# Performance work log

Measured on AMD Instinct MI355X. Metric: run time of the kernel, lower is better.

## Reference

```python
import jax, jax.numpy as jnp
import numpy as np

B, S, D = 4, 2048, 1024
H = 16
HD = D // H  # head dim = 64


def setup_inputs() -> dict:
    key = jax.random.key(0)
    ks = jax.random.split(key, 9)
    s = 1.0 / np.sqrt(D)
    return {
        "Q": jax.random.normal(ks[0], (B, S, D), dtype=jnp.float32),
        "K": jax.random.normal(ks[1], (B, S, D), dtype=jnp.float32),
        "V": jax.random.normal(ks[2], (B, S, D), dtype=jnp.float32),
        "Wq": jax.random.uniform(ks[3], (D, D), jnp.float32, -s, s),
        "bq": jax.random.uniform(ks[4], (D,), jnp.float32, -s, s),
        "Wk": jax.random.uniform(ks[5], (D, D), jnp.float32, -s, s),
        "bk": jax.random.uniform(ks[6], (D,), jnp.float32, -s, s),
        "Wv": jax.random.uniform(ks[7], (D, D), jnp.float32, -s, s),
        "bv": jax.random.uniform(ks[8], (D,), jnp.float32, -s, s),
    }


def reference(Q, K, V, Wq, bq, Wk, bk, Wv, bv):
    # Linear projections, split into heads: (B, H, S, HD)
    def proj(x, W, b):
        y = x @ W + b  # torch Linear uses x @ W.T; here W is stored pre-transposed (D_in, D_out)
        return y.reshape(B, S, H, HD).transpose(0, 2, 1, 3)

    q = proj(Q, Wq, bq)
    k = proj(K, Wk, bk)
    v = proj(V, Wv, bv)

    scale = 1.0 / jnp.sqrt(jnp.float32(HD))
    scores = jnp.einsum("bhqd,bhkd->bhqk", q, k) * scale  # (B,H,S,S)
    # causal mask (mask=True path): -inf above the diagonal
    causal = jnp.triu(jnp.full((S, S), -jnp.inf, dtype=scores.dtype), k=1)
    scores = scores + causal
    attn = jax.nn.softmax(scores, axis=-1)
    ctx = jnp.einsum("bhqk,bhkd->bhqd", attn, v)  # (B,H,S,HD)
    return ctx.transpose(0, 2, 1, 3).reshape(B, S, H * HD)
```

## Files before the change

kernel.cpp:

```cpp
#include <hip/hip_runtime.h>
#include <hip/hip_bf16.h>
#include <stdint.h>

#define B_  4
#define S_  2048
#define D_  1024
#define H_  16
#define HD_ 64
#define LOG2E 1.44269504088896f

typedef unsigned short u16;
typedef short bf16x8 __attribute__((ext_vector_type(8)));
typedef float f32x4 __attribute__((ext_vector_type(4)));

static __device__ __forceinline__ u16 f2bf(float f) {
    union { float f; uint32_t u; } v; v.f = f;
    return (u16)((v.u + 0x7FFF + ((v.u >> 16) & 1)) >> 16);
}

static __device__ __forceinline__ uint32_t cvt_pk_bf16(float lo, float hi) {
    uint32_t r;
    asm("v_cvt_pk_bf16_f32 %0, %1, %2" : "=v"(r) : "v"(lo), "v"(hi));
    return r;
}

static __device__ __forceinline__ uint32_t pk2(float lo, float hi) {
    return __builtin_amdgcn_perm(__float_as_uint(hi), __float_as_uint(lo), 0x07060302u);
}

static __device__ __forceinline__ bf16x8 rd_swz(const u16* base, int row, int slot) {
    return *(const bf16x8*)((const char*)base + row * 128 + ((slot ^ (row & 7)) << 4));
}

static __device__ __forceinline__ void gll_swz(const u16* grow0, size_t stride,
                                               u16* lds_chunk, int lane) {
    const int r = lane >> 3;
    const int slot = (lane & 7) ^ r;
    const u16* g = grow0 + (size_t)r * stride + slot * 8;
    __builtin_amdgcn_global_load_lds(
        (const __attribute__((address_space(1))) uint32_t*)g,
        (__attribute__((address_space(3))) uint32_t*)lds_chunk, 16, 0, 0);
}

__global__ __launch_bounds__(256) void wtrans(
    const float* __restrict__ W0, const float* __restrict__ W1, const float* __restrict__ W2,
    u16* __restrict__ T0, u16* __restrict__ T1, u16* __restrict__ T2)
{
    const float* W = blockIdx.z == 0 ? W0 : (blockIdx.z == 1 ? W1 : W2);
    u16* T       = blockIdx.z == 0 ? T0 : (blockIdx.z == 1 ? T1 : T2);
    __shared__ float t[32][33];
    const int n0 = blockIdx.x * 32, k0 = blockIdx.y * 32;
    const int tx = threadIdx.x, ty = threadIdx.y;
#pragma unroll
    for (int i = 0; i < 4; ++i)
        t[ty + i * 8][tx] = W[(size_t)(k0 + ty + i * 8) * D_ + n0 + tx];
    __syncthreads();
#pragma unroll
    for (int i = 0; i < 4; ++i)
        T[(size_t)(n0 + ty + i * 8) * D_ + k0 + tx] = f2bf(t[tx][ty + i * 8]);
}

template <int MODE>
__global__ __launch_bounds__(256) void proj_gemm(
    const float* __restrict__ X, const u16* __restrict__ Wt,
    const float* __restrict__ bias, u16* __restrict__ out)
{
    __shared__ __align__(16) u16 lA[2][128 * 64];
    __shared__ __align__(16) u16 lB[2][128 * 64];
    const int tid = threadIdx.x;
    const int m0 = blockIdx.x * 128, n0 = blockIdx.y * 128;
    const int w = tid >> 6, lane = tid & 63;
    const int lr = lane & 15, lg = lane >> 4;
    const int wr = (w >> 1) * 64, wc = (w & 1) * 64;

    f32x4 acc[4][4] = {};
    float4 areg[8];

    auto loadA = [&](int k0) {
#pragma unroll
        for (int i = 0; i < 4; ++i) {
            const int lin = (i * 256 + tid) * 8;
            const int r = lin >> 6, c = lin & 63;
            const float* p = X + (size_t)(m0 + r) * D_ + k0 + c;
            areg[2 * i]     = *(const float4*)p;
            areg[2 * i + 1] = *(const float4*)(p + 4);
        }
    };
    auto writeA = [&](u16* dst) {
#pragma unroll
        for (int i = 0; i < 4; ++i) {
            const int lin = (i * 256 + tid) * 8;
            const int r = lin >> 6, c = lin & 63;
            uint4 pk;
            pk.x = pk2(areg[2 * i].x,     areg[2 * i].y);
            pk.y = pk2(areg[2 * i].z,     areg[2 * i].w);
            pk.z = pk2(areg[2 * i + 1].x, areg[2 * i + 1].y);
            pk.w = pk2(areg[2 * i + 1].z, areg[2 * i + 1].w);
            const int phys = r * 128 + (((c >> 3) ^ (r & 7)) << 4);
            *(uint4*)((char*)dst + phys) = pk;
        }
    };
    auto stageB = [&](int k0, u16* dst) {
#pragma unroll
        for (int i = 0; i < 4; ++i) {
            const int c = w * 4 + i;
            gll_swz(Wt + (size_t)(n0 + c * 8) * D_ + k0, D_, dst + c * 512, lane);
        }
    };
    auto mfmaStep = [&](const u16* A, const u16* Bb) {
#pragma unroll
        for (int kk = 0; kk < 2; ++kk) {
            bf16x8 af[4], bfr[4];
#pragma unroll
            for (int m = 0; m < 4; ++m)
                af[m] = rd_swz(A, wr + m * 16 + lr, kk * 4 + lg);
#pragma unroll
            for (int n = 0; n < 4; ++n)
                bfr[n] = rd_swz(Bb, wc + n * 16 + lr, kk * 4 + lg);
#pragma unroll
            for (int m = 0; m < 4; ++m)
#pragma unroll
                for (int n = 0; n < 4; ++n)
                    acc[m][n] = __builtin_amdgcn_mfma_f32_16x16x32_bf16(af[m], bfr[n], acc[m][n], 0, 0, 0);
        }
    };

    loadA(0);
    stageB(0, lB[0]);
    writeA(lA[0]);
    __syncthreads();

    for (int k0 = 0, s = 0; k0 < D_; k0 += 64, s ^= 1) {
        const int nk = k0 + 64;
        if (nk < D_) {
            loadA(nk);
            stageB(nk, lB[s ^ 1]);
        }
        mfmaStep(lA[s], lB[s]);
        if (nk < D_) writeA(lA[s ^ 1]);
        __syncthreads();
    }

#pragma unroll
    for (int m = 0; m < 4; ++m)
#pragma unroll
        for (int n = 0; n < 4; ++n)
#pragma unroll
            for (int j = 0; j < 4; ++j) {
                const int gm = m0 + wr + m * 16 + lg * 4 + j;
                const int gn = n0 + wc + n * 16 + lr;
                float y = acc[m][n][j] + bias[gn];
                if (MODE == 0) y *= 0.125f * LOG2E;
                const int bb = gm >> 11, s2 = gm & (S_ - 1);
                const int h = gn >> 6, hd = gn & 63;
                size_t off;
                if (MODE < 2) off = (((size_t)bb * H_ + h) * S_ + s2) * HD_ + hd;
                else {
                    const int s6 = s2 & 63;
                    const int sp = (s2 & ~63) | (s6 & 0x20) | ((s6 & 0xC) << 1) |
                                   ((s6 & 0x10) >> 2) | (s6 & 3);
                    off = (((size_t)bb * H_ + h) * HD_ + hd) * S_ + sp;
                }
                out[off] = f2bf(y);
            }
}

__global__ __launch_bounds__(512) void attn_kernel(
    const u16* __restrict__ qb, const u16* __restrict__ kb,
    const u16* __restrict__ vtb, float* __restrict__ out)
{
    const int bh = blockIdx.y;
    const int b = bh >> 4, h = bh & 15;
    const int tid = threadIdx.x;
    const int w = tid >> 6, lane = tid & 63;
    const int lr = lane & 15, lg = lane >> 4;

    __shared__ __align__(16) u16 lds[2][4][64 * 64];

    const size_t kbase = (size_t)bh * S_ * HD_;
    const size_t vbase = (size_t)bh * HD_ * S_;

    union { uint32_t u[4]; bf16x8 v; } onesf;
    onesf.u[0] = onesf.u[1] = onesf.u[2] = onesf.u[3] = 0x3F803F80u;

    for (int e = 0; e < 2; ++e) {
        const int qi = (e == 0) ? (int)blockIdx.x : 15 - (int)blockIdx.x;
        const int q0 = qi * 128;
        const int qrow = q0 + w * 16 + lr;

        const size_t qoff = ((size_t)bh * S_ + qrow) * HD_;
        const bf16x8 qf0 = *(const bf16x8*)(qb + qoff + lg * 8);
        const bf16x8 qf1 = *(const bf16x8*)(qb + qoff + 32 + lg * 8);

        f32x4 oacc[4] = {};
        f32x4 lacc = {};

        const int tmax = 2 * qi + 1;

        auto stage = [&](int tp, int s) {
            const int kvA = tp * 64, kvB = kvA + 64;
            u16* d = &lds[s][0][0];
            gll_swz(kb + kbase + (size_t)(kvA + w * 8) * HD_, HD_, d + w * 512, lane);
            gll_swz(vtb + vbase + (size_t)(w * 8) * S_ + kvA, S_, d + 4096 + w * 512, lane);
            gll_swz(kb + kbase + (size_t)(kvB + w * 8) * HD_, HD_, d + 8192 + w * 512, lane);
            gll_swz(vtb + vbase + (size_t)(w * 8) * S_ + kvB, S_, d + 12288 + w * 512, lane);
        };

        auto compute = [&](int t, const u16* lK, const u16* lV) {
            const int kv0 = t * 64;
            f32x4 sacc[4];
            __builtin_amdgcn_s_setprio(1);
#pragma unroll
            for (int n = 0; n < 4; ++n) {
                const bf16x8 k0f = rd_swz(lK, n * 16 + lr, lg);
                const bf16x8 k1f = rd_swz(lK, n * 16 + lr, 4 + lg);
                f32x4 z = {};
                z = __builtin_amdgcn_mfma_f32_16x16x32_bf16(k0f, qf0, z, 0, 0, 0);
                z = __builtin_amdgcn_mfma_f32_16x16x32_bf16(k1f, qf1, z, 0, 0, 0);
                sacc[n] = z;
            }
            __builtin_amdgcn_s_setprio(0);

            if (t >= tmax - 1) {
#pragma unroll
                for (int n = 0; n < 4; ++n)
#pragma unroll
                    for (int j = 0; j < 4; ++j)
                        if (kv0 + n * 16 + lg * 4 + j > qrow) sacc[n][j] = -1e30f;
            }

            uint32_t pw[4][2];
#pragma unroll
            for (int n = 0; n < 4; ++n)
#pragma unroll
                for (int jh = 0; jh < 2; ++jh)
                    pw[n][jh] = cvt_pk_bf16(exp2f(sacc[n][2 * jh]),
                                            exp2f(sacc[n][2 * jh + 1]));

            union { uint32_t u[4]; bf16x8 v; } a0, a1;
            a0.u[0] = pw[0][0]; a0.u[1] = pw[0][1];
            a0.u[2] = pw[1][0]; a0.u[3] = pw[1][1];
            a1.u[0] = pw[2][0]; a1.u[1] = pw[2][1];
            a1.u[2] = pw[3][0]; a1.u[3] = pw[3][1];

            __builtin_amdgcn_s_setprio(1);
#pragma unroll
            for (int n = 0; n < 4; ++n) {
                const int row = n * 16 + lr;
                const bf16x8 vf0 = rd_swz(lV, row, lg);
                const bf16x8 vf1 = rd_swz(lV, row, 4 + lg);
                oacc[n] = __builtin_amdgcn_mfma_f32_16x16x32_bf16(a0.v, vf0, oacc[n], 0, 0, 0);
                oacc[n] = __builtin_amdgcn_mfma_f32_16x16x32_bf16(a1.v, vf1, oacc[n], 0, 0, 0);
            }
            lacc = __builtin_amdgcn_mfma_f32_16x16x32_bf16(a0.v, onesf.v, lacc, 0, 0, 0);
            lacc = __builtin_amdgcn_mfma_f32_16x16x32_bf16(a1.v, onesf.v, lacc, 0, 0, 0);
            __builtin_amdgcn_s_setprio(0);
        };

        stage(0, 0);
        __syncthreads();

        for (int tp = 0, s = 0; tp <= tmax; tp += 2, s ^= 1) {
            if (tp + 2 <= tmax) stage(tp + 2, s ^ 1);
            const u16* base = &lds[s][0][0];
            compute(tp, base, base + 4096);
            if (!(tp + 1 == tmax && w < 4)) compute(tp + 1, base + 8192, base + 12288);
            __syncthreads();
        }

        f32x4 inv;
#pragma unroll
        for (int j = 0; j < 4; ++j) inv[j] = 1.f / lacc[j];
#pragma unroll
        for (int j = 0; j < 4; ++j) {
            const int row = q0 + w * 16 + lg * 4 + j;
#pragma unroll
            for (int n = 0; n < 4; ++n)
                out[((size_t)b * S_ + row) * D_ + h * HD_ + n * 16 + lr] = oacc[n][j] * inv[j];
        }
    }
}

extern "C" void kernel_launch(void* const* d_in, const int* in_sizes, int n_in,
                              void* d_out, int out_size, void* d_ws, size_t ws_size,
                              hipStream_t stream) {
    const float* Q  = (const float*)d_in[0];
    const float* K  = (const float*)d_in[1];
    const float* V  = (const float*)d_in[2];
    const float* Wq = (const float*)d_in[3];
    const float* bq = (const float*)d_in[4];
    const float* Wk = (const float*)d_in[5];
    const float* bk = (const float*)d_in[6];
    const float* Wv = (const float*)d_in[7];
    const float* bv = (const float*)d_in[8];
    float* out = (float*)d_out;

    char* ws = (char*)d_ws;
    const size_t WT_BYTES  = (size_t)D_ * D_ * 2;
    const size_t QKV_BYTES = (size_t)B_ * S_ * D_ * 2;
    u16* Wtq = (u16*)(ws);
    u16* Wtk = (u16*)(ws + WT_BYTES);
    u16* Wtv = (u16*)(ws + 2 * WT_BYTES);
    u16* qb  = (u16*)(ws + 3 * WT_BYTES);
    u16* kb  = (u16*)(ws + 3 * WT_BYTES + QKV_BYTES);
    u16* vtb = (u16*)(ws + 3 * WT_BYTES + 2 * QKV_BYTES);

    wtrans<<<dim3(32, 32, 3), dim3(32, 8), 0, stream>>>(Wq, Wk, Wv, Wtq, Wtk, Wtv);
    proj_gemm<0><<<dim3(64, 8), dim3(256), 0, stream>>>(Q, Wtq, bq, qb);
    proj_gemm<1><<<dim3(64, 8), dim3(256), 0, stream>>>(K, Wtk, bk, kb);
    proj_gemm<2><<<dim3(64, 8), dim3(256), 0, stream>>>(V, Wtv, bv, vtb);
    attn_kernel<<<dim3(8, B_ * H_), dim3(512), 0, stream>>>(qb, kb, vtb, out);
}
```

Measured before the change: 150.6 us.

## Share K/V tile loads between both paired query tiles in one pass

Instead of processing the two paired causal query tiles (qi and 15-qi) sequentially, each reloading K/V from global memory, the kernel now streams K/V once up to the longer tile's range and applies each staged tile to both query tiles. This removes the redundant K/V staging for the shorter tile and halves the number of load/sync loop passes. The cost is doubled accumulator registers (two sets of output and row-sum accumulators plus Q fragments), which may raise register pressure and reduce occupancy.

```diff
diff --git a/kernel.cpp b/kernel.cpp
--- a/kernel.cpp
+++ b/kernel.cpp
@@ -183,100 +183,126 @@
     union { uint32_t u[4]; bf16x8 v; } onesf;
     onesf.u[0] = onesf.u[1] = onesf.u[2] = onesf.u[3] = 0x3F803F80u;
 
-    for (int e = 0; e < 2; ++e) {
-        const int qi = (e == 0) ? (int)blockIdx.x : 15 - (int)blockIdx.x;
-        const int q0 = qi * 128;
-        const int qrow = q0 + w * 16 + lr;
-
-        const size_t qoff = ((size_t)bh * S_ + qrow) * HD_;
-        const bf16x8 qf0 = *(const bf16x8*)(qb + qoff + lg * 8);
-        const bf16x8 qf1 = *(const bf16x8*)(qb + qoff + 32 + lg * 8);
-
-        f32x4 oacc[4] = {};
-        f32x4 lacc = {};
-
-        const int tmax = 2 * qi + 1;
-
-        auto stage = [&](int tp, int s) {
-            const int kvA = tp * 64, kvB = kvA + 64;
-            u16* d = &lds[s][0][0];
-            gll_swz(kb + kbase + (size_t)(kvA + w * 8) * HD_, HD_, d + w * 512, lane);
-            gll_swz(vtb + vbase + (size_t)(w * 8) * S_ + kvA, S_, d + 4096 + w * 512, lane);
-            gll_swz(kb + kbase + (size_t)(kvB + w * 8) * HD_, HD_, d + 8192 + w * 512, lane);
-            gll_swz(vtb + vbase + (size_t)(w * 8) * S_ + kvB, S_, d + 12288 + w * 512, lane);
-        };
-
-        auto compute = [&](int t, const u16* lK, const u16* lV) {
-            const int kv0 = t * 64;
-            f32x4 sacc[4];
-            __builtin_amdgcn_s_setprio(1);
-#pragma unroll
-            for (int n = 0; n < 4; ++n) {
-                const bf16x8 k0f = rd_swz(lK, n * 16 + lr, lg);
-                const bf16x8 k1f = rd_swz(lK, n * 16 + lr, 4 + lg);
-                f32x4 z = {};
-                z = __builtin_amdgcn_mfma_f32_16x16x32_bf16(k0f, qf0, z, 0, 0, 0);
-                z = __builtin_amdgcn_mfma_f32_16x16x32_bf16(k1f, qf1, z, 0, 0, 0);
-                sacc[n] = z;
-            }
-            __builtin_amdgcn_s_setprio(0);
-
-            if (t >= tmax - 1) {
-#pragma unroll
-                for (int n = 0; n < 4; ++n)
-#pragma unroll
-                    for (int j = 0; j < 4; ++j)
-                        if (kv0 + n * 16 + lg * 4 + j > qrow) sacc[n][j] = -1e30f;
-            }
-
-            uint32_t pw[4][2];
+    const int qA = (int)blockIdx.x;
+    const int qB = 15 - qA;
+    const int q0A = qA * 128, q0B = qB * 128;
+    const int qrowA = q0A + w * 16 + lr;
+    const int qrowB = q0B + w * 16 + lr;
+    const int tmaxA = 2 * qA + 1, tmaxB = 2 * qB + 1;
+
+    const size_t qoffA = ((size_t)bh * S_ + qrowA) * HD_;
+    const size_t qoffB = ((size_t)bh * S_ + qrowB) * HD_;
+    const bf16x8 qfA0 = *(const bf16x8*)(qb + qoffA + lg * 8);
+    const bf16x8 qfA1 = *(const bf16x8*)(qb + qoffA + 32 + lg * 8);
+    const bf16x8 qfB0 = *(const bf16x8*)(qb + qoffB + lg * 8);
+    const bf16x8 qfB1 = *(const bf16x8*)(qb + qoffB + 32 + lg * 8);
+
+    f32x4 oaccA[4] = {}, oaccB[4] = {};
+    f32x4 laccA = {}, laccB = {};
+
+    auto stage = [&](int tp, int s) {
+        const int kvA = tp * 64, kvB = kvA + 64;
+        u16* d = &lds[s][0][0];
+        gll_swz(kb + kbase + (size_t)(kvA + w * 8) * HD_, HD_, d + w * 512, lane);
+        gll_swz(vtb + vbase + (size_t)(w * 8) * S_ + kvA, S_, d + 4096 + w * 512, lane);
+        gll_swz(kb + kbase + (size_t)(kvB + w * 8) * HD_, HD_, d + 8192 + w * 512, lane);
+        gll_swz(vtb + vbase + (size_t)(w * 8) * S_ + kvB, S_, d + 12288 + w * 512, lane);
+    };
+
+    auto computeT = [&](int t, const u16* lK, const u16* lV,
+                        const bf16x8& Qf0, const bf16x8& Qf1,
+                        f32x4 (&oacc)[4], f32x4& lacc, int qrow, int tmax) {
+        const int kv0 = t * 64;
+        f32x4 sacc[4];
+        __builtin_amdgcn_s_setprio(1);
+#pragma unroll
+        for (int n = 0; n < 4; ++n) {
+            const bf16x8 k0f = rd_swz(lK, n * 16 + lr, lg);
+            const bf16x8 k1f = rd_swz(lK, n * 16 + lr, 4 + lg);
+            f32x4 z = {};
+            z = __builtin_amdgcn_mfma_f32_16x16x32_bf16(k0f, Qf0, z, 0, 0, 0);
+            z = __builtin_amdgcn_mfma_f32_16x16x32_bf16(k1f, Qf1, z, 0, 0, 0);
+            sacc[n] = z;
+        }
+        __builtin_amdgcn_s_setprio(0);
+
+        if (t >= tmax - 1) {
 #pragma unroll
             for (int n = 0; n < 4; ++n)
 #pragma unroll
-                for (int jh = 0; jh < 2; ++jh)
-                    pw[n][jh] = cvt_pk_bf16(exp2f(sacc[n][2 * jh]),
-                                            exp2f(sacc[n][2 * jh + 1]));
-
-            union { uint32_t u[4]; bf16x8 v; } a0, a1;
-            a0.u[0] = pw[0][0]; a0.u[1] = pw[0][1];
-            a0.u[2] = pw[1][0]; a0.u[3] = pw[1][1];
-            a1.u[0] = pw[2][0]; a1.u[1] = pw[2][1];
-            a1.u[2] = pw[3][0]; a1.u[3] = pw[3][1];
-
-            __builtin_amdgcn_s_setprio(1);
-#pragma unroll
-            for (int n = 0; n < 4; ++n) {
-                const int row = n * 16 + lr;
-                const bf16x8 vf0 = rd_swz(lV, row, lg);
-                const bf16x8 vf1 = rd_swz(lV, row, 4 + lg);
-                oacc[n] = __builtin_amdgcn_mfma_f32_16x16x32_bf16(a0.v, vf0, oacc[n], 0, 0, 0);
-                oacc[n] = __builtin_amdgcn_mfma_f32_16x16x32_bf16(a1.v, vf1, oacc[n], 0, 0, 0);
-            }
-            lacc = __builtin_amdgcn_mfma_f32_16x16x32_bf16(a0.v, onesf.v, lacc, 0, 0, 0);
-            lacc = __builtin_amdgcn_mfma_f32_16x16x32_bf16(a1.v, onesf.v, lacc, 0, 0, 0);
-            __builtin_amdgcn_s_setprio(0);
-        };
-
-        stage(0, 0);
+                for (int j = 0; j < 4; ++j)
+                    if (kv0 + n * 16 + lg * 4 + j > qrow) sacc[n][j] = -1e30f;
+        }
+
+        uint32_t pw[4][2];
+#pragma unroll
+        for (int n = 0; n < 4; ++n)
+#pragma unroll
+            for (int jh = 0; jh < 2; ++jh)
+                pw[n][jh] = cvt_pk_bf16(exp2f(sacc[n][2 * jh]),
+                                        exp2f(sacc[n][2 * jh + 1]));
+
+        union { uint32_t u[4]; bf16x8 v; } a0, a1;
+        a0.u[0] = pw[0][0]; a0.u[1] = pw[0][1];
+        a0.u[2] = pw[1][0]; a0.u[3] = pw[1][1];
+        a1.u[0] = pw[2][0]; a1.u[1] = pw[2][1];
+        a1.u[2] = pw[3][0]; a1.u[3] = pw[3][1];
+
+        __builtin_amdgcn_s_setprio(1);
+#pragma unroll
+        for (int n = 0; n < 4; ++n) {
+            const int row = n * 16 + lr;
+            const bf16x8 vf0 = rd_swz(lV, row, lg);
+            const bf16x8 vf1 = rd_swz(lV, row, 4 + lg);
+            oacc[n] = __builtin_amdgcn_mfma_f32_16x16x32_bf16(a0.v, vf0, oacc[n], 0, 0, 0);
+            oacc[n] = __builtin_amdgcn_mfma_f32_16x16x32_bf16(a1.v, vf1, oacc[n], 0, 0, 0);
+        }
+        lacc = __builtin_amdgcn_mfma_f32_16x16x32_bf16(a0.v, onesf.v, lacc, 0, 0, 0);
+        lacc = __builtin_amdgcn_mfma_f32_16x16x32_bf16(a1.v, onesf.v, lacc, 0, 0, 0);
+        __builtin_amdgcn_s_setprio(0);
+    };
+
+    stage(0, 0);
+    __syncthreads();
+
+    for (int tp = 0, s = 0; tp <= tmaxB; tp += 2, s ^= 1) {
+        if (tp + 2 <= tmaxB) stage(tp + 2, s ^ 1);
+        const u16* base = &lds[s][0][0];
+
+        computeT(tp, base, base + 4096, qfB0, qfB1, oaccB, laccB, qrowB, tmaxB);
+        if (!(tp + 1 == tmaxB && w < 4))
+            computeT(tp + 1, base + 8192, base + 12288, qfB0, qfB1, oaccB, laccB, qrowB, tmaxB);
+
+        if (tp <= tmaxA) {
+            computeT(tp, base, base + 4096, qfA0, qfA1, oaccA, laccA, qrowA, tmaxA);
+            if (!(tp + 1 == tmaxA && w < 4))
+                computeT(tp + 1, base + 8192, base + 12288, qfA0, qfA1, oaccA, laccA, qrowA, tmaxA);
+        }
         __syncthreads();
-
-        for (int tp = 0, s = 0; tp <= tmax; tp += 2, s ^= 1) {
-            if (tp + 2 <= tmax) stage(tp + 2, s ^ 1);
-            const u16* base = &lds[s][0][0];
-            compute(tp, base, base + 4096);
-            if (!(tp + 1 == tmax && w < 4)) compute(tp + 1, base + 8192, base + 12288);
-            __syncthreads();
-        }
-
+    }
+
+    {
         f32x4 inv;
 #pragma unroll
-        for (int j = 0; j < 4; ++j) inv[j] = 1.f / lacc[j];
+        for (int j = 0; j < 4; ++j) inv[j] = 1.f / laccA[j];
 #pragma unroll
         for (int j = 0; j < 4; ++j) {
-            const int row = q0 + w * 16 + lg * 4 + j;
+            const int row = q0A + w * 16 + lg * 4 + j;
 #pragma unroll
             for (int n = 0; n < 4; ++n)
-                out[((size_t)b * S_ + row) * D_ + h * HD_ + n * 16 + lr] = oacc[n][j] * inv[j];
+                out[((size_t)b * S_ + row) * D_ + h * HD_ + n * 16 + lr] = oaccA[n][j] * inv[j];
+        }
+    }
+    {
+        f32x4 inv;
+#pragma unroll
+        for (int j = 0; j < 4; ++j) inv[j] = 1.f / laccB[j];
+#pragma unroll
+        for (int j = 0; j < 4; ++j) {
+            const int row = q0B + w * 16 + lg * 4 + j;
+#pragma unroll
+            for (int n = 0; n < 4; ++n)
+                out[((size_t)b * S_ + row) * D_ + h * HD_ + n * 16 + lr] = oaccB[n][j] * inv[j];
         }
     }
 }
```

After: 147.4 us. 1.02x faster.
